# Kernel tuning notes

Hardware: AMD Instinct MI355X
Metric: run time of the kernel (lower is better)

Reference implementation:

```python
import jax, jax.numpy as jnp
import numpy as np

N_NODES = 100000
N_EDGES = 1600000
IN_DIM = 256
OUT_DIM = 64
LEAKY_SLOPE = 0.01  # torch F.leaky_relu default


def setup_inputs() -> dict:
    key = jax.random.key(0)
    k1, k2, k3, k4, k5 = jax.random.split(key, 5)
    h = jax.random.normal(k1, (N_NODES, IN_DIM), dtype=jnp.float32)
    W_fc = jax.random.normal(k2, (IN_DIM, OUT_DIM), dtype=jnp.float32) * (1.0 / np.sqrt(IN_DIM))
    a_attn = jax.random.normal(k3, (2 * OUT_DIM,), dtype=jnp.float32) * (1.0 / np.sqrt(2 * OUT_DIM))
    edge_src = jax.random.randint(k4, (N_EDGES,), 0, N_NODES, dtype=jnp.int32)
    edge_dst = jax.random.randint(k5, (N_EDGES,), 0, N_NODES, dtype=jnp.int32)
    return {"h": h, "W_fc": W_fc, "a_attn": a_attn, "edge_src": edge_src, "edge_dst": edge_dst}


def reference(h, W_fc, a_attn, edge_src, edge_dst):
    # z = fc(h)  (no bias)
    z = h @ W_fc                                   # [N, D]
    # edge attention: leaky_relu(concat(z_src, z_dst) @ a)
    # split a into src/dst halves -> node-level projections (same math, no concat)
    el = z @ a_attn[:OUT_DIM]                      # [N]
    er = z @ a_attn[OUT_DIM:]                      # [N]
    e = jax.nn.leaky_relu(el[edge_src] + er[edge_dst], negative_slope=LEAKY_SLOPE)  # [E]
    # segment softmax over destination-node mailboxes
    m = jax.ops.segment_max(e, edge_dst, num_segments=N_NODES)   # [N]
    ex = jnp.exp(e - m[edge_dst])                                # [E]
    s = jax.ops.segment_sum(ex, edge_dst, num_segments=N_NODES)  # [N]
    alpha = ex / s[edge_dst]                                     # [E]
    # weighted scatter-sum of neighbor features
    h_out = jax.ops.segment_sum(alpha[:, None] * z[edge_src], edge_dst, num_segments=N_NODES)  # [N, D]
    # heads != 1 branch: ELU (dropout = 0 in eval)
    return jax.nn.elu(h_out)
```

## Files before the change

kernel.cpp:

```cpp
#include <hip/hip_runtime.h>
#include <hip/hip_bf16.h>

#define IN_DIM 256
#define OUT_DIM 64
#define CHUNK 8192
#define BSH 8
#define P2CAP 6144

typedef short bf16x8 __attribute__((ext_vector_type(8)));
typedef float f32x4 __attribute__((ext_vector_type(4)));

__device__ inline unsigned short f2bf(float x) {
  unsigned int u = __float_as_uint(x);
  return (unsigned short)((u + 0x7FFFu + ((u >> 16) & 1u)) >> 16);
}

#define GLOAD_LDS16(gp, lp)                                                        \
  __builtin_amdgcn_global_load_lds(                                                \
      (const __attribute__((address_space(1))) unsigned int*)(gp),                 \
      (__attribute__((address_space(3))) unsigned int*)(lp), 16, 0, 0)

__global__ __launch_bounds__(256) void k_prep(const float* __restrict__ W,
                                              unsigned short* __restrict__ Wbf,
                                              int* __restrict__ tot) {
  int f = blockIdx.x * 256 + threadIdx.x;
  if (f < 512) tot[f] = 0;
  int kc = f >> 8, ct = (f >> 6) & 3, q = (f >> 4) & 3, nq = f & 15;
  int col = ct * 16 + nq, k0 = kc * 32 + q * 8;
  unsigned short v[8];
#pragma unroll
  for (int j = 0; j < 8; ++j) v[j] = f2bf(W[(size_t)(k0 + j) * OUT_DIM + col]);
  *(uint4*)(Wbf + (size_t)f * 8) = *(uint4*)v;
}

__global__ __launch_bounds__(256) void k_gemm(const float* __restrict__ h,
                                              const unsigned short* __restrict__ Wbf,
                                              const float* __restrict__ a,
                                              unsigned short* __restrict__ zb,
                                              float* __restrict__ el,
                                              float* __restrict__ er, int n,
                                              const int* __restrict__ dst,
                                              int* __restrict__ tot, int E,
                                              int nbuck) {
  __shared__ __align__(16) float Af[64 * 256];
  __shared__ int hist[512];
  const int t = threadIdx.x;
  const int base = blockIdx.x * 64;
  const int w = t >> 6, lane = t & 63, nq = lane & 15, q = lane >> 4;

  bf16x8 wf[8][4];
#pragma unroll
  for (int kc = 0; kc < 8; ++kc)
#pragma unroll
    for (int ct = 0; ct < 4; ++ct)
      wf[kc][ct] = *(const bf16x8*)(Wbf + (((kc * 4 + ct) * 64 + lane) << 3));

#pragma unroll
  for (int i = 0; i < 16; ++i) {
    int f = i * 256 + t;
    int row = f >> 6;
    int cb = (f & 63) * 16;
    int gcb = cb ^ ((row & 7) << 4);
    int grow = base + row;
    const char* gp = (grow < n) ? (const char*)h + ((size_t)grow * 1024 + gcb)
                                : (const char*)h;
    char* lp = (char*)Af + (size_t)(i * 4096 + w * 1024);
    GLOAD_LDS16(gp, lp);
  }
  __syncthreads();

  f32x4 acc[4];
#pragma unroll
  for (int ct = 0; ct < 4; ++ct) acc[ct] = (f32x4){0.f, 0.f, 0.f, 0.f};

  const int rowb = w * 16 + nq;
  const char* Arow = (const char*)Af + rowb * 1024;
  const int sw = (rowb & 7) << 4;

#pragma unroll
  for (int kc = 0; kc < 8; ++kc) {
    int c0 = kc * 128 + q * 32;
    float4 lo = *(const float4*)(Arow + (c0 ^ sw));
    float4 hi = *(const float4*)(Arow + ((c0 + 16) ^ sw));
    bf16x8 af;
    af[0] = (short)f2bf(lo.x); af[1] = (short)f2bf(lo.y);
    af[2] = (short)f2bf(lo.z); af[3] = (short)f2bf(lo.w);
    af[4] = (short)f2bf(hi.x); af[5] = (short)f2bf(hi.y);
    af[6] = (short)f2bf(hi.z); af[7] = (short)f2bf(hi.w);
#pragma unroll
    for (int ct = 0; ct < 4; ++ct)
      acc[ct] = __builtin_amdgcn_mfma_f32_16x16x32_bf16(af, wf[kc][ct], acc[ct], 0, 0, 0);
  }

  float a1[4], a2[4];
#pragma unroll
  for (int ct = 0; ct < 4; ++ct) {
    a1[ct] = a[ct * 16 + nq];
    a2[ct] = a[OUT_DIM + ct * 16 + nq];
  }
#pragma unroll
  for (int r = 0; r < 4; ++r) {
    int orow = base + w * 16 + q * 4 + r;
    float p1 = 0.f, p2 = 0.f;
#pragma unroll
    for (int ct = 0; ct < 4; ++ct) {
      float v = acc[ct][r];
      p1 += v * a1[ct];
      p2 += v * a2[ct];
      if (orow < n) zb[(size_t)orow * OUT_DIM + ct * 16 + nq] = f2bf(v);
    }
    p1 += __shfl_xor(p1, 1); p1 += __shfl_xor(p1, 2);
    p1 += __shfl_xor(p1, 4); p1 += __shfl_xor(p1, 8);
    p2 += __shfl_xor(p2, 1); p2 += __shfl_xor(p2, 2);
    p2 += __shfl_xor(p2, 4); p2 += __shfl_xor(p2, 8);
    if (orow < n && nq == 0) { el[orow] = p1; er[orow] = p2; }
  }

  hist[t] = 0;
  hist[t + 256] = 0;
  __syncthreads();
  int e0 = blockIdx.x * 1024 + t * 4;
  if (e0 + 4 <= E) {
    int4 d4 = *(const int4*)(dst + e0);
    atomicAdd(&hist[d4.x >> BSH], 1);
    atomicAdd(&hist[d4.y >> BSH], 1);
    atomicAdd(&hist[d4.z >> BSH], 1);
    atomicAdd(&hist[d4.w >> BSH], 1);
  } else {
#pragma unroll
    for (int k = 0; k < 4; ++k) {
      int e = e0 + k;
      if (e < E) atomicAdd(&hist[dst[e] >> BSH], 1);
    }
  }
  __syncthreads();
  for (int i = t; i < nbuck; i += 256)
    if (hist[i]) atomicAdd(&tot[i], hist[i]);
}

__global__ __launch_bounds__(256) void k_scanT(const int* __restrict__ tot,
                                               int* __restrict__ pbeg,
                                               int* __restrict__ gcur, int nbuck) {
  __shared__ int wtot[4];
  int t = threadIdx.x;
  int d0 = (2 * t < nbuck) ? tot[2 * t] : 0;
  int d1 = (2 * t + 1 < nbuck) ? tot[2 * t + 1] : 0;
  int tsum = d0 + d1;
  int lane = t & 63, w = t >> 6;
  int incl = tsum;
  for (int o = 1; o < 64; o <<= 1) {
    int u = __shfl_up(incl, o);
    if (lane >= o) incl += u;
  }
  if (lane == 63) wtot[w] = incl;
  __syncthreads();
  int woff = 0;
  for (int i = 0; i < 4; ++i)
    if (i < w) woff += wtot[i];
  int ex = woff + incl - tsum;
  pbeg[2 * t] = ex;
  gcur[2 * t] = ex;
  pbeg[2 * t + 1] = ex + d0;
  gcur[2 * t + 1] = ex + d0;
}

__global__ __launch_bounds__(512) void k_part(const int* __restrict__ src,
                                              const int* __restrict__ dst,
                                              int* __restrict__ gcur,
                                              int* __restrict__ pairs, int E,
                                              int nbuck) {
  __shared__ int hist[512];
  __shared__ int excl[512];
  __shared__ int cur[512];
  __shared__ int rbase[512];
  __shared__ int stage[CHUNK];
  __shared__ unsigned short sbk[CHUNK];
  __shared__ int wtot[8];
  const int t = threadIdx.x, b = blockIdx.x;
  const int beg = b * CHUNK;
  const int cnt = min(CHUNK, E - beg);

  hist[t] = 0;
  __syncthreads();

  int dv[16], sv[16];
#pragma unroll
  for (int k = 0; k < 16; ++k) {
    int i = k * 512 + t;
    dv[k] = -1;
    if (i < cnt) {
      dv[k] = dst[beg + i];
      sv[k] = src[beg + i];
      atomicAdd(&hist[dv[k] >> BSH], 1);
    }
  }
  __syncthreads();

  {
    int v = hist[t];
    int lane = t & 63, w = t >> 6;
    int incl = v;
    for (int o = 1; o < 64; o <<= 1) {
      int u = __shfl_up(incl, o);
      if (lane >= o) incl += u;
    }
    if (lane == 63) wtot[w] = incl;
    __syncthreads();
    int woff = 0;
    for (int i = 0; i < 8; ++i)
      if (i < w) woff += wtot[i];
    int ex = woff + incl - v;
    excl[t] = ex;
    cur[t] = ex;
    if (t < nbuck && v > 0) rbase[t] = atomicAdd(&gcur[t], v);
  }
  __syncthreads();

#pragma unroll
  for (int k = 0; k < 16; ++k) {
    if (dv[k] >= 0) {
      int bk = dv[k] >> BSH;
      int r = atomicAdd(&cur[bk], 1);
      stage[r] = ((dv[k] & ((1 << BSH) - 1)) << 24) | sv[k];
      sbk[r] = (unsigned short)bk;
    }
  }
  __syncthreads();

  for (int i = t; i < cnt; i += 512) {
    int bk = sbk[i];
    pairs[rbase[bk] + (i - excl[bk])] = stage[i];
  }
}

__global__ __launch_bounds__(1024) void k_p2agg(const int* __restrict__ pairs,
                                                const int* __restrict__ tot,
                                                const int* __restrict__ pbeg,
                                                const float* __restrict__ el,
                                                const float* __restrict__ er,
                                                const unsigned short* __restrict__ zb,
                                                float* __restrict__ out, int n) {
  __shared__ int deg[256];
  __shared__ int loff[257];
  __shared__ int cur[256];
  __shared__ int stage[P2CAP];
  __shared__ int wtot[4];
  const int t = threadIdx.x, b = blockIdx.x;
  const int beg = pbeg[b];
  const int cnt = tot[b];

  if (t < 256) deg[t] = 0;
  __syncthreads();

  int pv[6];
#pragma unroll
  for (int k = 0; k < 6; ++k) {
    int i = k * 1024 + t;
    pv[k] = 0;
    if (i < cnt) {
      pv[k] = pairs[beg + i];
      atomicAdd(&deg[((unsigned)pv[k]) >> 24], 1);
    }
  }
  __syncthreads();

  int v = 0, inc = 0;
  const int lane = t & 63, w = t >> 6;
  if (t < 256) {
    v = deg[t];
    inc = v;
    for (int o = 1; o < 64; o <<= 1) {
      int u = __shfl_up(inc, o);
      if (lane >= o) inc += u;
    }
    if (lane == 63) wtot[w] = inc;
  }
  __syncthreads();
  if (t < 256) {
    int woff = 0;
    for (int i = 0; i < 4; ++i)
      if (i < w) woff += wtot[i];
    int ex = woff + inc - v;
    loff[t] = ex;
    cur[t] = ex;
    if (t == 255) loff[256] = ex + v;
  }
  __syncthreads();

#pragma unroll
  for (int k = 0; k < 6; ++k) {
    int i = k * 1024 + t;
    if (i < cnt) {
      int r = atomicAdd(&cur[((unsigned)pv[k]) >> 24], 1);
      if (r < P2CAP) stage[r] = pv[k] & 0xFFFFFF;
    }
  }
  __syncthreads();

  const int g = t >> 4;
  const int cq = (t & 15) * 4;
#pragma unroll
  for (int round = 0; round < 4; ++round) {
    int nl = round * 64 + g;
    int node = (b << BSH) + nl;
    if (node >= n) continue;
    int jb = loff[nl], je = loff[nl + 1];
    float erd = er[node];
    float ax = 0.f, ay = 0.f, az = 0.f, aw = 0.f, ssum = 0.f;
    int j = jb;
    for (; j + 4 <= je; j += 4) {
      int s0 = stage[j], s1 = stage[j + 1], s2 = stage[j + 2], s3 = stage[j + 3];
      uint2 z0 = *(const uint2*)(zb + (s0 << 6) + cq);
      uint2 z1 = *(const uint2*)(zb + (s1 << 6) + cq);
      uint2 z2 = *(const uint2*)(zb + (s2 << 6) + cq);
      uint2 z3 = *(const uint2*)(zb + (s3 << 6) + cq);
      float x0 = el[s0] + erd, x1 = el[s1] + erd;
      float x2 = el[s2] + erd, x3 = el[s3] + erd;
      x0 = x0 > 0.f ? x0 : 0.01f * x0;
      x1 = x1 > 0.f ? x1 : 0.01f * x1;
      x2 = x2 > 0.f ? x2 : 0.01f * x2;
      x3 = x3 > 0.f ? x3 : 0.01f * x3;
      float e0 = __expf(x0), e1 = __expf(x1), e2 = __expf(x2), e3 = __expf(x3);
      ssum += (e0 + e1) + (e2 + e3);
      ax += e0 * __uint_as_float(z0.x << 16) + e1 * __uint_as_float(z1.x << 16) +
            e2 * __uint_as_float(z2.x << 16) + e3 * __uint_as_float(z3.x << 16);
      ay += e0 * __uint_as_float(z0.x & 0xFFFF0000u) + e1 * __uint_as_float(z1.x & 0xFFFF0000u) +
            e2 * __uint_as_float(z2.x & 0xFFFF0000u) + e3 * __uint_as_float(z3.x & 0xFFFF0000u);
      az += e0 * __uint_as_float(z0.y << 16) + e1 * __uint_as_float(z1.y << 16) +
            e2 * __uint_as_float(z2.y << 16) + e3 * __uint_as_float(z3.y << 16);
      aw += e0 * __uint_as_float(z0.y & 0xFFFF0000u) + e1 * __uint_as_float(z1.y & 0xFFFF0000u) +
            e2 * __uint_as_float(z2.y & 0xFFFF0000u) + e3 * __uint_as_float(z3.y & 0xFFFF0000u);
    }
    for (; j < je; ++j) {
      int s = stage[j];
      uint2 zv = *(const uint2*)(zb + (s << 6) + cq);
      float x = el[s] + erd;
      x = x > 0.f ? x : 0.01f * x;
      float ex = __expf(x);
      ssum += ex;
      ax += ex * __uint_as_float(zv.x << 16);
      ay += ex * __uint_as_float(zv.x & 0xFFFF0000u);
      az += ex * __uint_as_float(zv.y << 16);
      aw += ex * __uint_as_float(zv.y & 0xFFFF0000u);
    }
    float4 o = make_float4(0.f, 0.f, 0.f, 0.f);
    if (je > jb) {
      float inv = 1.f / ssum;
      ax *= inv; ay *= inv; az *= inv; aw *= inv;
      o.x = ax > 0.f ? ax : __expf(ax) - 1.f;
      o.y = ay > 0.f ? ay : __expf(ay) - 1.f;
      o.z = az > 0.f ? az : __expf(az) - 1.f;
      o.w = aw > 0.f ? aw : __expf(aw) - 1.f;
    }
    *(float4*)(out + ((size_t)node << 6) + cq) = o;
  }
}

extern "C" void kernel_launch(void* const* d_in, const int* in_sizes, int n_in,
                              void* d_out, int out_size, void* d_ws, size_t ws_size,
                              hipStream_t stream) {
  const float* h = (const float*)d_in[0];
  const float* W = (const float*)d_in[1];
  const float* a = (const float*)d_in[2];
  const int* src = (const int*)d_in[3];
  const int* dst = (const int*)d_in[4];
  const int n = in_sizes[0] / IN_DIM;
  const int E = in_sizes[3];
  float* out = (float*)d_out;

  const int b1 = (E + CHUNK - 1) / CHUNK;
  const int nbuck = (n + (1 << BSH) - 1) >> BSH;

  char* ws = (char*)d_ws;
  auto alloc = [&](size_t bytes) {
    char* p = ws;
    ws += (bytes + 15) & ~(size_t)15;
    return p;
  };
  unsigned short* Wbf = (unsigned short*)alloc(16384 * 2);
  unsigned short* zb = (unsigned short*)alloc((size_t)n * OUT_DIM * 2);
  float* el = (float*)alloc((size_t)n * 4);
  float* er = (float*)alloc((size_t)n * 4);
  int* tot = (int*)alloc(512 * 4);
  int* pbeg = (int*)alloc(512 * 4);
  int* gcur = (int*)alloc(512 * 4);
  int* pairs = (int*)alloc((size_t)E * 4);

  k_prep<<<8, 256, 0, stream>>>(W, Wbf, tot);
  k_gemm<<<(n + 63) / 64, 256, 0, stream>>>(h, Wbf, a, zb, el, er, n, dst, tot, E, nbuck);
  k_scanT<<<1, 256, 0, stream>>>(tot, pbeg, gcur, nbuck);
  k_part<<<b1, 512, 0, stream>>>(src, dst, gcur, pairs, E, nbuck);
  k_p2agg<<<nbuck, 1024, 0, stream>>>(pairs, tot, pbeg, el, er, zb, out, n);
}
```

Measured before the change: 242.4 us.

## Make GEMM kernel persistent with double-buffered LDS prefetch of h tiles

Turns the projection GEMM into a persistent kernel with 256 blocks that loop over row tiles. While computing the current tile, each block prefetches the next tile into a second LDS buffer using async global-to-LDS loads, so memory latency overlaps with MFMA work. The W fragments are also loaded once per block instead of once per tile. The edge histogram is repartitioned across the fixed grid. Doubling LDS to 128KB limits the kernel to one block per CU, so latency hiding now rests entirely on the prefetch.

```diff
diff --git a/kernel.cpp b/kernel.cpp
--- a/kernel.cpp
+++ b/kernel.cpp
@@ -33,20 +33,21 @@
   *(uint4*)(Wbf + (size_t)f * 8) = *(uint4*)v;
 }
 
-__global__ __launch_bounds__(256) void k_gemm(const float* __restrict__ h,
-                                              const unsigned short* __restrict__ Wbf,
-                                              const float* __restrict__ a,
-                                              unsigned short* __restrict__ zb,
-                                              float* __restrict__ el,
-                                              float* __restrict__ er, int n,
-                                              const int* __restrict__ dst,
-                                              int* __restrict__ tot, int E,
-                                              int nbuck) {
-  __shared__ __align__(16) float Af[64 * 256];
+__global__ __launch_bounds__(256, 1) void k_gemm(const float* __restrict__ h,
+                                                 const unsigned short* __restrict__ Wbf,
+                                                 const float* __restrict__ a,
+                                                 unsigned short* __restrict__ zb,
+                                                 float* __restrict__ el,
+                                                 float* __restrict__ er, int n,
+                                                 const int* __restrict__ dst,
+                                                 int* __restrict__ tot, int E,
+                                                 int nbuck) {
+  __shared__ __align__(16) float Af[2][64 * 256];
   __shared__ int hist[512];
   const int t = threadIdx.x;
-  const int base = blockIdx.x * 64;
   const int w = t >> 6, lane = t & 63, nq = lane & 15, q = lane >> 4;
+  const int nt = (n + 63) >> 6;
+  const int G = gridDim.x;
 
   bf16x8 wf[8][4];
 #pragma unroll
@@ -54,43 +55,6 @@
 #pragma unroll
     for (int ct = 0; ct < 4; ++ct)
       wf[kc][ct] = *(const bf16x8*)(Wbf + (((kc * 4 + ct) * 64 + lane) << 3));
-
-#pragma unroll
-  for (int i = 0; i < 16; ++i) {
-    int f = i * 256 + t;
-    int row = f >> 6;
-    int cb = (f & 63) * 16;
-    int gcb = cb ^ ((row & 7) << 4);
-    int grow = base + row;
-    const char* gp = (grow < n) ? (const char*)h + ((size_t)grow * 1024 + gcb)
-                                : (const char*)h;
-    char* lp = (char*)Af + (size_t)(i * 4096 + w * 1024);
-    GLOAD_LDS16(gp, lp);
-  }
-  __syncthreads();
-
-  f32x4 acc[4];
-#pragma unroll
-  for (int ct = 0; ct < 4; ++ct) acc[ct] = (f32x4){0.f, 0.f, 0.f, 0.f};
-
-  const int rowb = w * 16 + nq;
-  const char* Arow = (const char*)Af + rowb * 1024;
-  const int sw = (rowb & 7) << 4;
-
-#pragma unroll
-  for (int kc = 0; kc < 8; ++kc) {
-    int c0 = kc * 128 + q * 32;
-    float4 lo = *(const float4*)(Arow + (c0 ^ sw));
-    float4 hi = *(const float4*)(Arow + ((c0 + 16) ^ sw));
-    bf16x8 af;
-    af[0] = (short)f2bf(lo.x); af[1] = (short)f2bf(lo.y);
-    af[2] = (short)f2bf(lo.z); af[3] = (short)f2bf(lo.w);
-    af[4] = (short)f2bf(hi.x); af[5] = (short)f2bf(hi.y);
-    af[6] = (short)f2bf(hi.z); af[7] = (short)f2bf(hi.w);
-#pragma unroll
-    for (int ct = 0; ct < 4; ++ct)
-      acc[ct] = __builtin_amdgcn_mfma_f32_16x16x32_bf16(af, wf[kc][ct], acc[ct], 0, 0, 0);
-  }
 
   float a1[4], a2[4];
 #pragma unroll
@@ -98,39 +62,99 @@
     a1[ct] = a[ct * 16 + nq];
     a2[ct] = a[OUT_DIM + ct * 16 + nq];
   }
-#pragma unroll
-  for (int r = 0; r < 4; ++r) {
-    int orow = base + w * 16 + q * 4 + r;
-    float p1 = 0.f, p2 = 0.f;
-#pragma unroll
-    for (int ct = 0; ct < 4; ++ct) {
-      float v = acc[ct][r];
-      p1 += v * a1[ct];
-      p2 += v * a2[ct];
-      if (orow < n) zb[(size_t)orow * OUT_DIM + ct * 16 + nq] = f2bf(v);
-    }
-    p1 += __shfl_xor(p1, 1); p1 += __shfl_xor(p1, 2);
-    p1 += __shfl_xor(p1, 4); p1 += __shfl_xor(p1, 8);
-    p2 += __shfl_xor(p2, 1); p2 += __shfl_xor(p2, 2);
-    p2 += __shfl_xor(p2, 4); p2 += __shfl_xor(p2, 8);
-    if (orow < n && nq == 0) { el[orow] = p1; er[orow] = p2; }
+
+  auto stage = [&](int bsel, int tile) {
+    const int base = tile << 6;
+#pragma unroll
+    for (int i = 0; i < 16; ++i) {
+      int f = i * 256 + t;
+      int row = f >> 6;
+      int cb = (f & 63) * 16;
+      int gcb = cb ^ ((row & 7) << 4);
+      int grow = base + row;
+      const char* gp = (grow < n) ? (const char*)h + ((size_t)grow * 1024 + gcb)
+                                  : (const char*)h;
+      char* lp = (char*)&Af[bsel][0] + (i * 4096 + w * 1024);
+      GLOAD_LDS16(gp, lp);
+    }
+  };
+
+  const int rowb = w * 16 + nq;
+  const int sw = (rowb & 7) << 4;
+
+  int cur = 0;
+  stage(0, blockIdx.x);
+  for (int tile = blockIdx.x; tile < nt; tile += G) {
+    int nxt = tile + G;
+    if (nxt < nt) {
+      stage(cur ^ 1, nxt);
+      asm volatile("s_waitcnt vmcnt(16)" ::: "memory");
+    } else {
+      asm volatile("s_waitcnt vmcnt(0)" ::: "memory");
+    }
+    __builtin_amdgcn_sched_barrier(0);
+    __builtin_amdgcn_s_barrier();
+
+    const char* Arow = (const char*)&Af[cur][0] + rowb * 1024;
+    f32x4 acc[4];
+#pragma unroll
+    for (int ct = 0; ct < 4; ++ct) acc[ct] = (f32x4){0.f, 0.f, 0.f, 0.f};
+#pragma unroll
+    for (int kc = 0; kc < 8; ++kc) {
+      int c0 = kc * 128 + q * 32;
+      float4 lo = *(const float4*)(Arow + (c0 ^ sw));
+      float4 hi = *(const float4*)(Arow + ((c0 + 16) ^ sw));
+      bf16x8 af;
+      af[0] = (short)f2bf(lo.x); af[1] = (short)f2bf(lo.y);
+      af[2] = (short)f2bf(lo.z); af[3] = (short)f2bf(lo.w);
+      af[4] = (short)f2bf(hi.x); af[5] = (short)f2bf(hi.y);
+      af[6] = (short)f2bf(hi.z); af[7] = (short)f2bf(hi.w);
+#pragma unroll
+      for (int ct = 0; ct < 4; ++ct)
+        acc[ct] = __builtin_amdgcn_mfma_f32_16x16x32_bf16(af, wf[kc][ct], acc[ct], 0, 0, 0);
+    }
+
+    const int base = tile << 6;
+#pragma unroll
+    for (int r = 0; r < 4; ++r) {
+      int orow = base + w * 16 + q * 4 + r;
+      float p1 = 0.f, p2 = 0.f;
+#pragma unroll
+      for (int ct = 0; ct < 4; ++ct) {
+        float v = acc[ct][r];
+        p1 += v * a1[ct];
+        p2 += v * a2[ct];
+        if (orow < n) zb[(size_t)orow * OUT_DIM + ct * 16 + nq] = f2bf(v);
+      }
+      p1 += __shfl_xor(p1, 1); p1 += __shfl_xor(p1, 2);
+      p1 += __shfl_xor(p1, 4); p1 += __shfl_xor(p1, 8);
+      p2 += __shfl_xor(p2, 1); p2 += __shfl_xor(p2, 2);
+      p2 += __shfl_xor(p2, 4); p2 += __shfl_xor(p2, 8);
+      if (orow < n && nq == 0) { el[orow] = p1; er[orow] = p2; }
+    }
+
+    asm volatile("s_waitcnt lgkmcnt(0)" ::: "memory");
+    __builtin_amdgcn_s_barrier();
+    cur ^= 1;
   }
 
   hist[t] = 0;
   hist[t + 256] = 0;
   __syncthreads();
-  int e0 = blockIdx.x * 1024 + t * 4;
-  if (e0 + 4 <= E) {
-    int4 d4 = *(const int4*)(dst + e0);
-    atomicAdd(&hist[d4.x >> BSH], 1);
-    atomicAdd(&hist[d4.y >> BSH], 1);
-    atomicAdd(&hist[d4.z >> BSH], 1);
-    atomicAdd(&hist[d4.w >> BSH], 1);
-  } else {
-#pragma unroll
-    for (int k = 0; k < 4; ++k) {
-      int e = e0 + k;
-      if (e < E) atomicAdd(&hist[dst[e] >> BSH], 1);
+  const int ER = (((E + G - 1) / G) + 3) & ~3;
+  const int ebeg = blockIdx.x * ER;
+  const int eend = min(E, ebeg + ER);
+  for (int e0 = ebeg + t * 4; e0 < eend; e0 += 1024) {
+    if (e0 + 4 <= eend) {
+      int4 d4 = *(const int4*)(dst + e0);
+      atomicAdd(&hist[d4.x >> BSH], 1);
+      atomicAdd(&hist[d4.y >> BSH], 1);
+      atomicAdd(&hist[d4.z >> BSH], 1);
+      atomicAdd(&hist[d4.w >> BSH], 1);
+    } else {
+#pragma unroll
+      for (int k = 0; k < 4; ++k)
+        if (e0 + k < eend) atomicAdd(&hist[dst[e0 + k] >> BSH], 1);
     }
   }
   __syncthreads();
@@ -387,7 +411,7 @@
   int* pairs = (int*)alloc((size_t)E * 4);
 
   k_prep<<<8, 256, 0, stream>>>(W, Wbf, tot);
-  k_gemm<<<(n + 63) / 64, 256, 0, stream>>>(h, Wbf, a, zb, el, er, n, dst, tot, E, nbuck);
+  k_gemm<<<256, 256, 0, stream>>>(h, Wbf, a, zb, el, er, n, dst, tot, E, nbuck);
   k_scanT<<<1, 256, 0, stream>>>(tot, pbeg, gcur, nbuck);
   k_part<<<b1, 512, 0, stream>>>(src, dst, gcur, pairs, E, nbuck);
   k_p2agg<<<nbuck, 1024, 0, stream>>>(pairs, tot, pbeg, el, er, zb, out, n);
```

Measured after the change: 242.0 us. No clear change (-0.2%).
